# Kernel optimization log

Hardware: AMD Instinct MI355X
Metric: run time of the kernel (lower is better)

Reference implementation:

```python
import jax, jax.numpy as jnp
import numpy as np

RADIUS = 0.2
NSAMPLE = 32
EPS = 1e-5  # BatchNorm2d default eps


def _bn_relu(x, g, b):
    # BatchNorm2d in training mode: per-channel stats over (B, S, nsample), biased var.
    m = x.mean(axis=(0, 1, 2))
    v = jnp.mean((x - m) ** 2, axis=(0, 1, 2))
    return jax.nn.relu((x - m) * jax.lax.rsqrt(v + EPS) * g + b)


def setup_inputs() -> dict:
    key = jax.random.key(0)
    ks = jax.random.split(key, 8)
    B, N, S = 8, 8192, 2048
    xyz = jax.random.uniform(ks[0], (B, 3, N), dtype=jnp.float32)          # unit cube
    points = jax.random.normal(ks[1], (B, 3, N), dtype=jnp.float32)
    fps_idx = jax.random.randint(ks[2], (B, S), 0, N, dtype=jnp.int32)
    W1 = jax.random.normal(ks[3], (64, 6), dtype=jnp.float32) * 0.1
    W2 = jax.random.normal(ks[4], (64, 64), dtype=jnp.float32) * 0.1
    W3 = jax.random.normal(ks[5], (128, 64), dtype=jnp.float32) * 0.1
    return dict(
        xyz=xyz, points=points, fps_idx=fps_idx,
        W1=W1, g1=jnp.ones((64,)), b1=jnp.zeros((64,)),
        W2=W2, g2=jnp.ones((64,)), b2=jnp.zeros((64,)),
        W3=W3, g3=jnp.ones((128,)), b3=jnp.zeros((128,)),
    )


def reference(xyz, points, fps_idx, W1, g1, b1, W2, g2, b2, W3, g3, b3):
    B, _, N = xyz.shape
    xyz_t = jnp.transpose(xyz, (0, 2, 1))            # [B,N,3]
    pts_t = jnp.transpose(points, (0, 2, 1))         # [B,N,D]
    # gather_operation: sampled centers
    new_xyz_t = jnp.take_along_axis(xyz_t, fps_idx[:, :, None], axis=1)  # [B,S,3]
    # ball query: first NSAMPLE points within radius; pad with first hit
    d2 = jnp.sum((new_xyz_t[:, :, None, :] - xyz_t[:, None, :, :]) ** 2, axis=-1)  # [B,S,N]
    keys = jnp.where(d2 <= RADIUS * RADIUS, jnp.arange(N, dtype=jnp.int32), N)
    neg_top, _ = jax.lax.top_k(-keys, NSAMPLE)       # smallest keys first
    idx = -neg_top                                   # [B,S,NSAMPLE]
    idx = jnp.where(idx < N, idx, idx[:, :, 0:1])    # pad empty slots with first hit (self always in-radius)
    bidx = jnp.arange(B)[:, None, None]
    grouped_xyz = xyz_t[bidx, idx]                   # [B,S,ns,3]
    rel = grouped_xyz - new_xyz_t[:, :, None, :]     # center-relative coords
    grouped_pts = pts_t[bidx, idx]                   # [B,S,ns,D]
    feat = jnp.concatenate([rel, grouped_pts], axis=-1)  # [B,S,ns,3+D]
    for W, g, b in ((W1, g1, b1), (W2, g2, b2), (W3, g3, b3)):
        feat = _bn_relu(jnp.einsum('bsnc,oc->bsno', feat, W), g, b)
    new_points = jnp.max(feat, axis=2)               # max over neighbors -> [B,S,C]
    return jnp.transpose(new_xyz_t, (0, 2, 1)), jnp.transpose(new_points, (0, 2, 1))
```

## Files before the change

kernel.cpp:

```cpp
#include <hip/hip_runtime.h>
#include <hip/hip_bf16.h>

#define BB_ 8
#define NN_ 8192
#define SS_ 2048
#define NS 32
#define C1 64
#define C2 64
#define C3 128
#define RAD2 0.04f
#define BN_EPS 1e-5f
#define M_TOT (BB_*SS_*NS)
#define INV_M (1.0f/524288.0f)
#define YSTR 34

typedef __attribute__((ext_vector_type(8))) short bf16x8;
typedef __attribute__((ext_vector_type(4))) float f32x4;

#define FBF_OFF 0
#define WPK_OFF 2097152
#define ST_OFF  2104320
#define GMM_OFF 2104832
#define X2_OFF  4201984
#define WS_NEED ((size_t)(4201984 + 16777216) * 4)

__device__ inline unsigned pkbf(float a, float b) {
    __hip_bfloat162 h = __float22bfloat162_rn(make_float2(a, b));
    unsigned r; __builtin_memcpy(&r, &h, 4); return r;
}
__device__ inline bf16x8 asfrag(uint4 v) { bf16x8 r; __builtin_memcpy(&r, &v, 16); return r; }
__device__ inline float bflo(unsigned u) { unsigned x = u << 16; float f; __builtin_memcpy(&f, &x, 4); return f; }
__device__ inline float bfhi(unsigned u) { unsigned x = u & 0xffff0000u; float f; __builtin_memcpy(&f, &x, 4); return f; }

__device__ inline void fin1_ch(const float* __restrict__ st, const float* __restrict__ W1,
                               const float* __restrict__ g, const float* __restrict__ bb,
                               int o, float* __restrict__ al, float* __restrict__ cl) {
    float w[6];
    #pragma unroll
    for (int i = 0; i < 6; ++i) w[i] = W1[o * 6 + i];
    float ms = 0.f;
    #pragma unroll
    for (int i = 0; i < 6; ++i) ms = fmaf(w[i], st[i], ms);
    float m = ms * INV_M;
    float e2 = 0.f;
    #pragma unroll
    for (int ci = 0; ci < 6; ++ci)
        #pragma unroll
        for (int d = 0; d < 6; ++d) {
            int lo = ci < d ? ci : d, hi = ci < d ? d : ci;
            int idx = 6 + lo * 6 - lo * (lo + 1) / 2 + hi;
            e2 = fmaf(w[ci] * w[d], st[idx], e2);
        }
    float var = e2 * INV_M - m * m;
    float ai = g[o] * (1.0f / sqrtf(var + BN_EPS));
    al[o] = ai;
    cl[o] = bb[o] - m * ai;
}

__device__ inline void fin_ch(const float* __restrict__ sum, const float* __restrict__ sq,
                              const float* __restrict__ g, const float* __restrict__ bb,
                              int o, float* __restrict__ al, float* __restrict__ cl) {
    float m = sum[o] * INV_M;
    float var = sq[o] * INV_M - m * m;
    float ai = g[o] * (1.0f / sqrtf(var + BN_EPS));
    al[o] = ai;
    cl[o] = bb[o] - m * ai;
}

__global__ void k_front(const float* __restrict__ xyz, const float* __restrict__ pts,
                        const int* __restrict__ fps, uint4* __restrict__ fbf,
                        const float* __restrict__ W1, const float* __restrict__ W2,
                        const float* __restrict__ W3, uint4* __restrict__ wf,
                        float* __restrict__ st) {
    __shared__ int lidx[4][NS];
    int tid = threadIdx.x;
    if (blockIdx.x >= 4096) {
        int bb = blockIdx.x - 4096;
        if (bb == 7) { st[tid] = 0.f; st[tid + 256] = 0.f; return; }
        int t = bb * 256 + tid;
        int l = t & 63, p = l & 15, qd = l >> 4;
        float v[8];
        if (t < 256) {
            int mt = t >> 6;
            #pragma unroll
            for (int j = 0; j < 8; ++j)
                v[j] = (qd == 0 && j < 6) ? W1[(mt * 16 + p) * 6 + j] : 0.f;
        } else if (t < 768) {
            int fr = (t - 256) >> 6;
            int mt = fr >> 1, kf = fr & 1;
            #pragma unroll
            for (int j = 0; j < 8; ++j)
                v[j] = W2[(16 * mt + p) * 64 + kf * 32 + qd * 8 + j];
        } else {
            int fr = (t - 768) >> 6;
            int nt = fr >> 1, kf = fr & 1;
            #pragma unroll
            for (int j = 0; j < 8; ++j)
                v[j] = W3[(nt * 16 + p) * 64 + kf * 32 + qd * 8 + j];
        }
        uint4 o;
        o.x = pkbf(v[0], v[1]); o.y = pkbf(v[2], v[3]);
        o.z = pkbf(v[4], v[5]); o.w = pkbf(v[6], v[7]);
        wf[t] = o;
        return;
    }
    int wave = (blockIdx.x * blockDim.x + tid) >> 6;
    int lane = tid & 63;
    int wslot = tid >> 6;
    int b = wave / SS_;
    const float* xb = xyz + (size_t)b * 3 * NN_;
    const float* pb = pts + (size_t)b * 3 * NN_;
    int ci = fps[wave];
    float cx = xb[ci], cy = xb[NN_ + ci], cz = xb[2 * NN_ + ci];

    float px = xb[lane], py = xb[NN_ + lane], pz = xb[2 * NN_ + lane];
    int found = 0;
    int first_i = -1;
    for (int base = 0; base < NN_; base += 64) {
        float xv = px, yv = py, zv = pz;
        int nb = (base + 64 < NN_) ? base + 64 : 0;
        px = xb[nb + lane]; py = xb[NN_ + nb + lane]; pz = xb[2 * NN_ + nb + lane];
        float dx = xv - cx, dy = yv - cy, dz = zv - cz;
        float d2 = __fadd_rn(__fadd_rn(__fmul_rn(dx, dx), __fmul_rn(dy, dy)), __fmul_rn(dz, dz));
        bool inr = d2 <= RAD2;
        unsigned long long mask = __ballot(inr);
        if (first_i < 0 && mask) first_i = base + __builtin_ctzll(mask);
        if (inr) {
            int pos = found + __popcll(mask & ((1ull << lane) - 1ull));
            if (pos < NS) lidx[wslot][pos] = base + lane;
        }
        found += __popcll(mask);
        if (found >= NS) break;
    }
    if (found > NS) found = NS;
    if (lane < NS) {
        int j = (lane < found) ? lidx[wslot][lane] : first_i;
        uint4 o;
        o.x = pkbf(xb[j] - cx,           xb[NN_ + j] - cy);
        o.y = pkbf(xb[2 * NN_ + j] - cz, pb[j]);
        o.z = pkbf(pb[NN_ + j],          pb[2 * NN_ + j]);
        o.w = 0u;
        fbf[(size_t)wave * NS + lane] = o;
    }
}

__global__ void k_p1(const uint4* __restrict__ fbf, float* __restrict__ st) {
    __shared__ float sacc[27];
    int tid = threadIdx.x;
    if (tid < 27) sacc[tid] = 0.f;
    __syncthreads();
    int gt = blockIdx.x * 256 + tid;
    float vals[27];
    #pragma unroll
    for (int i = 0; i < 27; ++i) vals[i] = 0.f;
    #pragma unroll 1
    for (int it = 0; it < M_TOT / 65536; ++it) {
        uint4 w = fbf[it * 65536 + gt];
        float f[6] = { bflo(w.x), bfhi(w.x), bflo(w.y), bfhi(w.y), bflo(w.z), bfhi(w.z) };
        #pragma unroll
        for (int c = 0; c < 6; ++c) vals[c] += f[c];
        int q = 6;
        #pragma unroll
        for (int c = 0; c < 6; ++c)
            #pragma unroll
            for (int d = c; d < 6; ++d) { vals[q] = fmaf(f[c], f[d], vals[q]); ++q; }
    }
    int lane = tid & 63;
    #pragma unroll
    for (int i = 0; i < 27; ++i) {
        float v = vals[i];
        #pragma unroll
        for (int d = 32; d; d >>= 1) v += __shfl_xor(v, d);
        if (lane == 0) atomicAdd(&sacc[i], v);
    }
    __syncthreads();
    if (tid < 27) atomicAdd(&st[tid], sacc[tid]);
}

__global__ __launch_bounds__(128) void k_p2(
        const uint4* __restrict__ fbf, const uint4* __restrict__ wpk,
        float* __restrict__ st,
        const float* __restrict__ W1, const float* __restrict__ g1, const float* __restrict__ b1,
        uint2* __restrict__ x2, int store_x2) {
    __shared__ unsigned yls[2][64 * YSTR];
    __shared__ float bs[C2], bq[C2];
    __shared__ float a1ls[C1], c1ls[C1];
    int tid = threadIdx.x, wslot = tid >> 6, lane = tid & 63;
    int p = lane & 15, qd = lane >> 4;
    if (tid < C2) { bs[tid] = 0.f; bq[tid] = 0.f; fin1_ch(st, W1, g1, b1, tid, a1ls, c1ls); }
    __syncthreads();
    const uint4* w1f = wpk;
    const uint4* w2f = wpk + 256;
    unsigned* my = yls[wslot];
    float s2[4][4], q2[4][4];
    #pragma unroll
    for (int i = 0; i < 4; ++i)
        #pragma unroll
        for (int r = 0; r < 4; ++r) { s2[i][r] = 0.f; q2[i][r] = 0.f; }

    #pragma unroll 1
    for (int it = 0; it < 2; ++it) {
        int tile = it * 4096 + blockIdx.x * 2 + wslot;
        int base = tile * 64;
        bf16x8 B1[4];
        #pragma unroll
        for (int nt = 0; nt < 4; ++nt) {
            uint4 v = make_uint4(0u, 0u, 0u, 0u);
            if (qd == 0) v = fbf[base + nt * 16 + p];
            B1[nt] = asfrag(v);
        }
        #pragma unroll
        for (int mt = 0; mt < 4; ++mt) {
            bf16x8 A = asfrag(w1f[mt * 64 + lane]);
            float4 av = *(const float4*)(a1ls + mt * 16 + qd * 4);
            float4 cv = *(const float4*)(c1ls + mt * 16 + qd * 4);
            #pragma unroll
            for (int nt = 0; nt < 4; ++nt) {
                f32x4 acc = {0.f, 0.f, 0.f, 0.f};
                acc = __builtin_amdgcn_mfma_f32_16x16x32_bf16(A, B1[nt], acc, 0, 0, 0);
                float y0 = fmaxf(fmaf(av.x, acc[0], cv.x), 0.f);
                float y1 = fmaxf(fmaf(av.y, acc[1], cv.y), 0.f);
                float y2 = fmaxf(fmaf(av.z, acc[2], cv.z), 0.f);
                float y3 = fmaxf(fmaf(av.w, acc[3], cv.w), 0.f);
                int a = (nt * 16 + p) * YSTR + mt * 8 + qd * 2;
                *(uint2*)&my[a] = make_uint2(pkbf(y0, y1), pkbf(y2, y3));
            }
        }
        __syncthreads();
        bf16x8 B2[4][2];
        #pragma unroll
        for (int nt = 0; nt < 4; ++nt)
            #pragma unroll
            for (int kf = 0; kf < 2; ++kf)
                B2[nt][kf] = asfrag(*(const uint4*)&my[(nt * 16 + p) * YSTR + kf * 16 + qd * 4]);
        #pragma unroll
        for (int mt = 0; mt < 4; ++mt) {
            f32x4 acc[4];
            #pragma unroll
            for (int nt = 0; nt < 4; ++nt) acc[nt] = (f32x4){0.f, 0.f, 0.f, 0.f};
            #pragma unroll
            for (int kf = 0; kf < 2; ++kf) {
                bf16x8 W = asfrag(w2f[(mt * 2 + kf) * 64 + lane]);
                #pragma unroll
                for (int nt = 0; nt < 4; ++nt)
                    acc[nt] = __builtin_amdgcn_mfma_f32_16x16x32_bf16(W, B2[nt][kf], acc[nt], 0, 0, 0);
            }
            if (store_x2) {
                #pragma unroll
                for (int nt = 0; nt < 4; ++nt)
                    x2[(size_t)(tile * 64 + nt * 16 + p) * 16 + mt * 4 + qd] =
                        make_uint2(pkbf(acc[nt][0], acc[nt][1]), pkbf(acc[nt][2], acc[nt][3]));
            }
            #pragma unroll
            for (int r = 0; r < 4; ++r) {
                float u0 = acc[0][r], u1 = acc[1][r], u2 = acc[2][r], u3 = acc[3][r];
                s2[mt][r] += (u0 + u1) + (u2 + u3);
                q2[mt][r] = fmaf(u0, u0, fmaf(u1, u1, fmaf(u2, u2, fmaf(u3, u3, q2[mt][r]))));
            }
        }
        __syncthreads();
    }
    #pragma unroll
    for (int mt = 0; mt < 4; ++mt)
        #pragma unroll
        for (int r = 0; r < 4; ++r) {
            float s = s2[mt][r], q = q2[mt][r];
            #pragma unroll
            for (int off = 1; off <= 8; off <<= 1) { s += __shfl_xor(s, off); q += __shfl_xor(q, off); }
            if (p == 0) {
                atomicAdd(&bs[mt * 16 + qd * 4 + r], s);
                atomicAdd(&bq[mt * 16 + qd * 4 + r], q);
            }
        }
    __syncthreads();
    if (tid < C2) { atomicAdd(&st[64 + tid], bs[tid]); atomicAdd(&st[128 + tid], bq[tid]); }
}

__global__ __launch_bounds__(256) void k_p3_l3(
        const uint2* __restrict__ x2, const uint4* __restrict__ wpk,
        float* __restrict__ st,
        const float* __restrict__ g2, const float* __restrict__ b2,
        const float* __restrict__ g3, float* __restrict__ gmm) {
    __shared__ uint4 w3ls[1024];
    __shared__ float bs[C3], bq[C3];
    __shared__ float a2ls[C2], c2ls[C2];
    int tid = threadIdx.x, wslot = tid >> 6, lane = tid & 63;
    int p = lane & 15, qd = lane >> 4;
    if (tid < 128) bs[tid] = 0.f; else bq[tid - 128] = 0.f;
    #pragma unroll
    for (int i = 0; i < 4; ++i) w3ls[i * 256 + tid] = wpk[768 + i * 256 + tid];
    if (tid < C2) fin_ch(st + 64, st + 128, g2, b2, tid, a2ls, c2ls);
    __syncthreads();
    const uint4* x2u4 = (const uint4*)x2;
    float a2r[2][8], c2r[2][8];
    #pragma unroll
    for (int kf = 0; kf < 2; ++kf)
        #pragma unroll
        for (int j = 0; j < 8; ++j) {
            a2r[kf][j] = a2ls[kf * 32 + qd * 8 + j];
            c2r[kf][j] = c2ls[kf * 32 + qd * 8 + j];
        }
    float gs3[8], gq3[8], va[8], vb[8];
    bool pos[8];
    #pragma unroll
    for (int i = 0; i < 8; ++i) {
        gs3[i] = 0.f; gq3[i] = 0.f; va[i] = -3.4e38f; vb[i] = -3.4e38f;
        pos[i] = g3[i * 16 + p] >= 0.f;
    }
    int tile = blockIdx.x * 4 + wslot;
    size_t pb = (size_t)tile * 64;

    uint4 c0 = x2u4[(pb + p) * 8 + qd];
    uint4 c1 = x2u4[(pb + p) * 8 + 4 + qd];
    #pragma unroll 1
    for (int mt = 0; mt < 4; ++mt) {
        uint4 n0 = c0, n1 = c1;
        if (mt < 3) {
            n0 = x2u4[(pb + (mt + 1) * 16 + p) * 8 + qd];
            n1 = x2u4[(pb + (mt + 1) * 16 + p) * 8 + 4 + qd];
        }
        bf16x8 A0, A1;
        {
            unsigned w0[4] = { c0.x, c0.y, c0.z, c0.w };
            unsigned w1[4] = { c1.x, c1.y, c1.z, c1.w };
            unsigned r0[4], r1[4];
            #pragma unroll
            for (int wi = 0; wi < 4; ++wi) {
                float lo0 = bflo(w0[wi]), hi0 = bfhi(w0[wi]);
                r0[wi] = pkbf(fmaxf(fmaf(a2r[0][2 * wi], lo0, c2r[0][2 * wi]), 0.f),
                              fmaxf(fmaf(a2r[0][2 * wi + 1], hi0, c2r[0][2 * wi + 1]), 0.f));
                float lo1 = bflo(w1[wi]), hi1 = bfhi(w1[wi]);
                r1[wi] = pkbf(fmaxf(fmaf(a2r[1][2 * wi], lo1, c2r[1][2 * wi]), 0.f),
                              fmaxf(fmaf(a2r[1][2 * wi + 1], hi1, c2r[1][2 * wi + 1]), 0.f));
            }
            uint4 t0 = make_uint4(r0[0], r0[1], r0[2], r0[3]);
            uint4 t1 = make_uint4(r1[0], r1[1], r1[2], r1[3]);
            A0 = asfrag(t0); A1 = asfrag(t1);
        }
        int g = mt >> 1;
        #pragma unroll
        for (int nt = 0; nt < 8; ++nt) {
            bf16x8 Wa = asfrag(w3ls[(nt * 2 + 0) * 64 + lane]);
            bf16x8 Wb = asfrag(w3ls[(nt * 2 + 1) * 64 + lane]);
            f32x4 acc = __builtin_amdgcn_mfma_f32_16x16x32_bf16(A0, Wa,
                            (f32x4){0.f, 0.f, 0.f, 0.f}, 0, 0, 0);
            acc = __builtin_amdgcn_mfma_f32_16x16x32_bf16(A1, Wb, acc, 0, 0, 0);
            float v0 = acc[0], v1 = acc[1], v2 = acc[2], v3 = acc[3];
            gs3[nt] += (v0 + v1) + (v2 + v3);
            gq3[nt] = fmaf(v0, v0, fmaf(v1, v1, fmaf(v2, v2, fmaf(v3, v3, gq3[nt]))));
            float mx = fmaxf(fmaxf(v0, v1), fmaxf(v2, v3));
            float mn = fminf(fminf(v0, v1), fminf(v2, v3));
            float vv = pos[nt] ? mx : -mn;
            if (g == 0) va[nt] = fmaxf(va[nt], vv);
            else        vb[nt] = fmaxf(vb[nt], vv);
        }
        c0 = n0; c1 = n1;
    }
    #pragma unroll
    for (int nt = 0; nt < 8; ++nt) {
        float x = va[nt], y = vb[nt];
        x = fmaxf(x, __shfl_xor(x, 16)); x = fmaxf(x, __shfl_xor(x, 32));
        y = fmaxf(y, __shfl_xor(y, 16)); y = fmaxf(y, __shfl_xor(y, 32));
        if (lane < 16) {
            gmm[(size_t)(tile * 2 + 0) * C3 + nt * 16 + lane] = x;
            gmm[(size_t)(tile * 2 + 1) * C3 + nt * 16 + lane] = y;
        }
    }
    #pragma unroll
    for (int nt = 0; nt < 8; ++nt) {
        float s = gs3[nt], q = gq3[nt];
        s += __shfl_xor(s, 16); s += __shfl_xor(s, 32);
        q += __shfl_xor(q, 16); q += __shfl_xor(q, 32);
        if (lane < 16) {
            atomicAdd(&bs[nt * 16 + lane], s);
            atomicAdd(&bq[nt * 16 + lane], q);
        }
    }
    __syncthreads();
    if (tid < C3) { atomicAdd(&st[192 + tid], bs[tid]); atomicAdd(&st[320 + tid], bq[tid]); }
}

__global__ __launch_bounds__(256) void k_p3_fused(
        const uint4* __restrict__ fbf, const uint4* __restrict__ wpk,
        float* __restrict__ st,
        const float* __restrict__ W1, const float* __restrict__ g1, const float* __restrict__ b1,
        const float* __restrict__ g2, const float* __restrict__ b2,
        const float* __restrict__ g3, float* __restrict__ gmm) {
    __shared__ unsigned yls[4][64 * YSTR];
    __shared__ uint4 w3ls[1024];
    __shared__ float bs[C3], bq[C3];
    __shared__ float a1ls[C1], c1ls[C1], a2ls[C2], c2ls[C2];
    int tid = threadIdx.x, wslot = tid >> 6, lane = tid & 63;
    int p = lane & 15, qd = lane >> 4;
    if (tid < 128) bs[tid] = 0.f; else bq[tid - 128] = 0.f;
    #pragma unroll
    for (int i = 0; i < 4; ++i) w3ls[i * 256 + tid] = wpk[768 + i * 256 + tid];
    if (tid < 64) fin1_ch(st, W1, g1, b1, tid, a1ls, c1ls);
    else if (tid < 128) fin_ch(st + 64, st + 128, g2, b2, tid - 64, a2ls, c2ls);
    __syncthreads();
    const uint4* w1f = wpk;
    const uint4* w2f = wpk + 256;
    unsigned* my = yls[wslot];
    float gs3[8], gq3[8];
    bool pos[8];
    #pragma unroll
    for (int i = 0; i < 8; ++i) { gs3[i] = 0.f; gq3[i] = 0.f; pos[i] = g3[i * 16 + p] >= 0.f; }

    #pragma unroll 1
    for (int it = 0; it < 2; ++it) {
        int tile = it * 4096 + blockIdx.x * 4 + wslot;
        int base = tile * 64;
        bf16x8 B1[4];
        #pragma unroll
        for (int nt = 0; nt < 4; ++nt) {
            uint4 v = make_uint4(0u, 0u, 0u, 0u);
            if (qd == 0) v = fbf[base + nt * 16 + p];
            B1[nt] = asfrag(v);
        }
        #pragma unroll
        for (int mt = 0; mt < 4; ++mt) {
            bf16x8 A = asfrag(w1f[mt * 64 + lane]);
            float4 av = *(const float4*)(a1ls + mt * 16 + qd * 4);
            float4 cv = *(const float4*)(c1ls + mt * 16 + qd * 4);
            #pragma unroll
            for (int nt = 0; nt < 4; ++nt) {
                f32x4 acc = {0.f, 0.f, 0.f, 0.f};
                acc = __builtin_amdgcn_mfma_f32_16x16x32_bf16(A, B1[nt], acc, 0, 0, 0);
                float y0 = fmaxf(fmaf(av.x, acc[0], cv.x), 0.f);
                float y1 = fmaxf(fmaf(av.y, acc[1], cv.y), 0.f);
                float y2 = fmaxf(fmaf(av.z, acc[2], cv.z), 0.f);
                float y3 = fmaxf(fmaf(av.w, acc[3], cv.w), 0.f);
                int a = (nt * 16 + p) * YSTR + mt * 8 + qd * 2;
                *(uint2*)&my[a] = make_uint2(pkbf(y0, y1), pkbf(y2, y3));
            }
        }
        __syncthreads();
        bf16x8 B2[4][2];
        #pragma unroll
        for (int nt = 0; nt < 4; ++nt)
            #pragma unroll
            for (int kf = 0; kf < 2; ++kf)
                B2[nt][kf] = asfrag(*(const uint4*)&my[(nt * 16 + p) * YSTR + kf * 16 + qd * 4]);
        __syncthreads();
        #pragma unroll
        for (int mt = 0; mt < 4; ++mt) {
            f32x4 acc[4];
            #pragma unroll
            for (int nt = 0; nt < 4; ++nt) acc[nt] = (f32x4){0.f, 0.f, 0.f, 0.f};
            #pragma unroll
            for (int kf = 0; kf < 2; ++kf) {
                bf16x8 W = asfrag(w2f[(mt * 2 + kf) * 64 + lane]);
                #pragma unroll
                for (int nt = 0; nt < 4; ++nt)
                    acc[nt] = __builtin_amdgcn_mfma_f32_16x16x32_bf16(W, B2[nt][kf], acc[nt], 0, 0, 0);
            }
            float4 av = *(const float4*)(a2ls + mt * 16 + qd * 4);
            float4 cv = *(const float4*)(c2ls + mt * 16 + qd * 4);
            #pragma unroll
            for (int nt = 0; nt < 4; ++nt) {
                float y0 = fmaxf(fmaf(av.x, acc[nt][0], cv.x), 0.f);
                float y1 = fmaxf(fmaf(av.y, acc[nt][1], cv.y), 0.f);
                float y2 = fmaxf(fmaf(av.z, acc[nt][2], cv.z), 0.f);
                float y3 = fmaxf(fmaf(av.w, acc[nt][3], cv.w), 0.f);
                int a = (nt * 16 + p) * YSTR + mt * 8 + qd * 2;
                *(uint2*)&my[a] = make_uint2(pkbf(y0, y1), pkbf(y2, y3));
            }
        }
        __syncthreads();
        bf16x8 A3[4][2];
        #pragma unroll
        for (int mt = 0; mt < 4; ++mt) {
            A3[mt][0] = asfrag(*(const uint4*)&my[(mt * 16 + p) * YSTR + qd * 4]);
            A3[mt][1] = asfrag(*(const uint4*)&my[(mt * 16 + p) * YSTR + 16 + qd * 4]);
        }
        __syncthreads();
        #pragma unroll
        for (int nt = 0; nt < 8; ++nt) {
            bf16x8 Wa = asfrag(w3ls[(nt * 2 + 0) * 64 + lane]);
            bf16x8 Wb = asfrag(w3ls[(nt * 2 + 1) * 64 + lane]);
            f32x4 acc[4];
            #pragma unroll
            for (int mt = 0; mt < 4; ++mt) {
                acc[mt] = __builtin_amdgcn_mfma_f32_16x16x32_bf16(A3[mt][0], Wa,
                            (f32x4){0.f, 0.f, 0.f, 0.f}, 0, 0, 0);
                acc[mt] = __builtin_amdgcn_mfma_f32_16x16x32_bf16(A3[mt][1], Wb, acc[mt], 0, 0, 0);
            }
            float s = 0.f, q = 0.f, va = 0.f, vb = 0.f;
            #pragma unroll
            for (int mt = 0; mt < 4; ++mt) {
                float v0 = acc[mt][0], v1 = acc[mt][1], v2 = acc[mt][2], v3 = acc[mt][3];
                s += (v0 + v1) + (v2 + v3);
                q = fmaf(v0, v0, fmaf(v1, v1, fmaf(v2, v2, fmaf(v3, v3, q))));
                float mx = fmaxf(fmaxf(v0, v1), fmaxf(v2, v3));
                float mn = fminf(fminf(v0, v1), fminf(v2, v3));
                float vv = pos[nt] ? mx : -mn;
                if (mt == 0) va = vv;
                else if (mt == 1) va = fmaxf(va, vv);
                else if (mt == 2) vb = vv;
                else vb = fmaxf(vb, vv);
            }
            gs3[nt] += s; gq3[nt] += q;
            va = fmaxf(va, __shfl_xor(va, 16)); va = fmaxf(va, __shfl_xor(va, 32));
            vb = fmaxf(vb, __shfl_xor(vb, 16)); vb = fmaxf(vb, __shfl_xor(vb, 32));
            if (lane < 16) {
                gmm[(size_t)(tile * 2 + 0) * C3 + nt * 16 + lane] = va;
                gmm[(size_t)(tile * 2 + 1) * C3 + nt * 16 + lane] = vb;
            }
        }
    }
    #pragma unroll
    for (int nt = 0; nt < 8; ++nt) {
        float s = gs3[nt], q = gq3[nt];
        s += __shfl_xor(s, 16); s += __shfl_xor(s, 32);
        q += __shfl_xor(q, 16); q += __shfl_xor(q, 32);
        if (lane < 16) {
            atomicAdd(&bs[nt * 16 + lane], s);
            atomicAdd(&bq[nt * 16 + lane], q);
        }
    }
    __syncthreads();
    if (tid < C3) { atomicAdd(&st[192 + tid], bs[tid]); atomicAdd(&st[320 + tid], bq[tid]); }
}

__global__ void k_outx(const float* __restrict__ gmm, const float* __restrict__ st,
                       const float* __restrict__ g3, const float* __restrict__ b3,
                       const float* __restrict__ xyz, const int* __restrict__ fps,
                       float* __restrict__ out) {
    __shared__ float T[C3][17];
    __shared__ float a3ls[C3], c3ls[C3];
    int blk = blockIdx.x, tid = threadIdx.x;
    if (blk < 1024) {
        if (tid < C3) fin_ch(st + 192, st + 320, g3, b3, tid, a3ls, c3ls);
        __syncthreads();
        int b = blk >> 7, s0 = (blk & 127) << 4;
        #pragma unroll
        for (int i = 0; i < 8; ++i) {
            int idx = i * 256 + tid;
            int sl = idx >> 7, o = idx & 127;
            float m = gmm[((size_t)(b * SS_ + s0 + sl)) * C3 + o];
            float a = a3ls[o];
            float v = (a >= 0.f) ? m : -m;
            T[o][sl] = fmaxf(fmaf(a, v, c3ls[o]), 0.f);
        }
        __syncthreads();
        int o = tid & 127, sh = tid >> 7;
        float* dst = out + (size_t)BB_ * 3 * SS_ + ((size_t)b * C3 + o) * SS_ + s0 + sh * 8;
        float4 w0, w1;
        w0.x = T[o][sh * 8 + 0]; w0.y = T[o][sh * 8 + 1];
        w0.z = T[o][sh * 8 + 2]; w0.w = T[o][sh * 8 + 3];
        w1.x = T[o][sh * 8 + 4]; w1.y = T[o][sh * 8 + 5];
        w1.z = T[o][sh * 8 + 6]; w1.w = T[o][sh * 8 + 7];
        *(float4*)dst = w0; *(float4*)(dst + 4) = w1;
    } else {
        int t = (blk - 1024) * 256 + tid;
        int b = t / (3 * SS_);
        int r = (t / SS_) % 3;
        int s = t % SS_;
        int ci = fps[b * SS_ + s];
        out[t] = xyz[((size_t)b * 3 + r) * NN_ + ci];
    }
}

extern "C" void kernel_launch(void* const* d_in, const int* in_sizes, int n_in,
                              void* d_out, int out_size, void* d_ws, size_t ws_size,
                              hipStream_t stream) {
    (void)in_sizes; (void)n_in; (void)out_size;
    const float* xyz = (const float*)d_in[0];
    const float* pts = (const float*)d_in[1];
    const int*   fps = (const int*)d_in[2];
    const float* W1 = (const float*)d_in[3];
    const float* g1 = (const float*)d_in[4];
    const float* b1 = (const float*)d_in[5];
    const float* W2 = (const float*)d_in[6];
    const float* g2 = (const float*)d_in[7];
    const float* b2 = (const float*)d_in[8];
    const float* W3 = (const float*)d_in[9];
    const float* g3 = (const float*)d_in[10];
    const float* b3 = (const float*)d_in[11];
    float* out = (float*)d_out;
    float* ws = (float*)d_ws;

    uint4* fbf = (uint4*)(ws + FBF_OFF);
    uint4* wpk = (uint4*)(ws + WPK_OFF);
    float* st  = ws + ST_OFF;
    float* gmm = ws + GMM_OFF;
    uint2* x2  = (uint2*)(ws + X2_OFF);
    int split = (ws_size >= WS_NEED) ? 1 : 0;

    k_front<<<4096 + 8, 256, 0, stream>>>(xyz, pts, fps, fbf, W1, W2, W3, wpk, st);
    k_p1<<<256, 256, 0, stream>>>(fbf, st);
    k_p2<<<2048, 128, 0, stream>>>(fbf, wpk, st, W1, g1, b1, x2, split);
    if (split)
        k_p3_l3<<<2048, 256, 0, stream>>>(x2, wpk, st, g2, b2, g3, gmm);
    else
        k_p3_fused<<<1024, 256, 0, stream>>>(fbf, wpk, st, W1, g1, b1, g2, b2, g3, gmm);
    k_outx<<<1024 + 192, 256, 0, stream>>>(gmm, st, g3, b3, xyz, fps, out);
}
```

Measured before the change: 261.1 us.

## Store layer-2 activations in MFMA fragment-ready layout via LDS staging

The layer-2 pre-activation output x2 is now staged through shared memory and written as fragment-ordered uint4 chunks, so each lane writes and later reads one contiguous 16-byte vector. Previously the stores were strided uint2 writes and k_p3_l3 did gathered reads. k_p2 also halves its grid and processes four tiles per block instead of two, which amortises the per-block stats setup and the atomics. The cost is extra LDS traffic and barriers per tile, plus lower parallelism from the smaller grid.

```diff
diff --git a/kernel.cpp b/kernel.cpp
--- a/kernel.cpp
+++ b/kernel.cpp
@@ -181,7 +181,7 @@
         const uint4* __restrict__ fbf, const uint4* __restrict__ wpk,
         float* __restrict__ st,
         const float* __restrict__ W1, const float* __restrict__ g1, const float* __restrict__ b1,
-        uint2* __restrict__ x2, int store_x2) {
+        uint4* __restrict__ x2a, int store_x2) {
     __shared__ unsigned yls[2][64 * YSTR];
     __shared__ float bs[C2], bq[C2];
     __shared__ float a1ls[C1], c1ls[C1];
@@ -199,8 +199,8 @@
         for (int r = 0; r < 4; ++r) { s2[i][r] = 0.f; q2[i][r] = 0.f; }
 
     #pragma unroll 1
-    for (int it = 0; it < 2; ++it) {
-        int tile = it * 4096 + blockIdx.x * 2 + wslot;
+    for (int it = 0; it < 4; ++it) {
+        int tile = it * 2048 + blockIdx.x * 2 + wslot;
         int base = tile * 64;
         bf16x8 B1[4];
         #pragma unroll
@@ -233,6 +233,7 @@
             #pragma unroll
             for (int kf = 0; kf < 2; ++kf)
                 B2[nt][kf] = asfrag(*(const uint4*)&my[(nt * 16 + p) * YSTR + kf * 16 + qd * 4]);
+        __syncthreads();
         #pragma unroll
         for (int mt = 0; mt < 4; ++mt) {
             f32x4 acc[4];
@@ -247,9 +248,11 @@
             }
             if (store_x2) {
                 #pragma unroll
-                for (int nt = 0; nt < 4; ++nt)
-                    x2[(size_t)(tile * 64 + nt * 16 + p) * 16 + mt * 4 + qd] =
-                        make_uint2(pkbf(acc[nt][0], acc[nt][1]), pkbf(acc[nt][2], acc[nt][3]));
+                for (int nt = 0; nt < 4; ++nt) {
+                    int a = (nt * 16 + p) * YSTR + mt * 8 + qd * 2;
+                    *(uint2*)&my[a] = make_uint2(pkbf(acc[nt][0], acc[nt][1]),
+                                                 pkbf(acc[nt][2], acc[nt][3]));
+                }
             }
             #pragma unroll
             for (int r = 0; r < 4; ++r) {
@@ -258,6 +261,16 @@
                 q2[mt][r] = fmaf(u0, u0, fmaf(u1, u1, fmaf(u2, u2, fmaf(u3, u3, q2[mt][r]))));
             }
         }
+        if (store_x2) {
+            __syncthreads();
+            #pragma unroll
+            for (int mtc = 0; mtc < 4; ++mtc)
+                #pragma unroll
+                for (int kf = 0; kf < 2; ++kf) {
+                    uint4 v = *(const uint4*)&my[(mtc * 16 + p) * YSTR + kf * 16 + qd * 4];
+                    x2a[((size_t)tile * 8 + mtc * 2 + kf) * 64 + lane] = v;
+                }
+        }
         __syncthreads();
     }
     #pragma unroll
@@ -277,7 +290,7 @@
 }
 
 __global__ __launch_bounds__(256) void k_p3_l3(
-        const uint2* __restrict__ x2, const uint4* __restrict__ wpk,
+        const uint4* __restrict__ x2a, const uint4* __restrict__ wpk,
         float* __restrict__ st,
         const float* __restrict__ g2, const float* __restrict__ b2,
         const float* __restrict__ g3, float* __restrict__ gmm) {
@@ -291,7 +304,6 @@
     for (int i = 0; i < 4; ++i) w3ls[i * 256 + tid] = wpk[768 + i * 256 + tid];
     if (tid < C2) fin_ch(st + 64, st + 128, g2, b2, tid, a2ls, c2ls);
     __syncthreads();
-    const uint4* x2u4 = (const uint4*)x2;
     float a2r[2][8], c2r[2][8];
     #pragma unroll
     for (int kf = 0; kf < 2; ++kf)
@@ -308,16 +320,16 @@
         pos[i] = g3[i * 16 + p] >= 0.f;
     }
     int tile = blockIdx.x * 4 + wslot;
-    size_t pb = (size_t)tile * 64;
-
-    uint4 c0 = x2u4[(pb + p) * 8 + qd];
-    uint4 c1 = x2u4[(pb + p) * 8 + 4 + qd];
+    size_t cb = (size_t)tile * 8;
+
+    uint4 c0 = x2a[(cb + 0) * 64 + lane];
+    uint4 c1 = x2a[(cb + 1) * 64 + lane];
     #pragma unroll 1
     for (int mt = 0; mt < 4; ++mt) {
         uint4 n0 = c0, n1 = c1;
         if (mt < 3) {
-            n0 = x2u4[(pb + (mt + 1) * 16 + p) * 8 + qd];
-            n1 = x2u4[(pb + (mt + 1) * 16 + p) * 8 + 4 + qd];
+            n0 = x2a[(cb + (mt + 1) * 2 + 0) * 64 + lane];
+            n1 = x2a[(cb + (mt + 1) * 2 + 1) * 64 + lane];
         }
         bf16x8 A0, A1;
         {
@@ -584,14 +596,14 @@
     uint4* wpk = (uint4*)(ws + WPK_OFF);
     float* st  = ws + ST_OFF;
     float* gmm = ws + GMM_OFF;
-    uint2* x2  = (uint2*)(ws + X2_OFF);
+    uint4* x2a = (uint4*)(ws + X2_OFF);
     int split = (ws_size >= WS_NEED) ? 1 : 0;
 
     k_front<<<4096 + 8, 256, 0, stream>>>(xyz, pts, fps, fbf, W1, W2, W3, wpk, st);
     k_p1<<<256, 256, 0, stream>>>(fbf, st);
-    k_p2<<<2048, 128, 0, stream>>>(fbf, wpk, st, W1, g1, b1, x2, split);
+    k_p2<<<1024, 128, 0, stream>>>(fbf, wpk, st, W1, g1, b1, x2a, split);
     if (split)
-        k_p3_l3<<<2048, 256, 0, stream>>>(x2, wpk, st, g2, b2, g3, gmm);
+        k_p3_l3<<<2048, 256, 0, stream>>>(x2a, wpk, st, g2, b2, g3, gmm);
     else
         k_p3_fused<<<1024, 256, 0, stream>>>(fbf, wpk, st, W1, g1, b1, g2, b2, g3, gmm);
     k_outx<<<1024 + 192, 256, 0, stream>>>(gmm, st, g3, b3, xyz, fps, out);
```

Result: faster. 247.5 us (-5.2%).
